# Performance work log

Measured on AMD Instinct MI355X. Metric: run time of the kernel, lower is better.

Reference implementation:

```python
import jax, jax.numpy as jnp
import numpy as np

B, T, DIM, DIM_EPS, H = 4, 1024, 2048, 2048, 16
HD = DIM // H        # 128, value head dim
HDE = DIM_EPS // H   # 128, q/k head dim


def setup_inputs() -> dict:
    key = jax.random.key(0)
    ks = jax.random.split(key, 6)
    s = 0.02
    # rotary frequencies as in llama-style precompute (theta=10000)
    inv_freq = 1.0 / (10000.0 ** (np.arange(0, HDE, 2, dtype=np.float32) / HDE))
    t = np.arange(T, dtype=np.float32)
    ang = np.outer(t, inv_freq)  # (T, HDE//2)
    return {
        "v": jax.random.normal(ks[0], (B, T, DIM), jnp.float32),
        "x_eps": jax.random.normal(ks[1], (B, T, DIM_EPS), jnp.float32),
        "freqs_cos": jnp.asarray(np.cos(ang)),
        "freqs_sin": jnp.asarray(np.sin(ang)),
        "W_eps_attn": jax.random.normal(ks[2], (DIM_EPS, 2 * DIM_EPS), jnp.float32) * s,
        "W_attn": jax.random.normal(ks[3], (DIM, DIM), jnp.float32) * s,
        "W_proj": jax.random.normal(ks[4], (DIM, DIM), jnp.float32) * s,
        "W_eps_proj": jax.random.normal(ks[5], (DIM_EPS, DIM_EPS), jnp.float32) * s,
    }


def _rope(x, cos, sin):
    # x: (B, T, H, HDE) -> complex-multiply by freqs_cis of shape (T, HDE//2)
    xr = x.reshape(*x.shape[:-1], -1, 2)
    x_re, x_im = xr[..., 0], xr[..., 1]
    c = cos[None, :, None, :]  # (1, T, 1, HDE//2)
    s = sin[None, :, None, :]
    o_re = x_re * c - x_im * s
    o_im = x_re * s + x_im * c
    return jnp.stack([o_re, o_im], axis=-1).reshape(x.shape)


def reference(v, x_eps, freqs_cos, freqs_sin, W_eps_attn, W_attn, W_proj, W_eps_proj):
    Bn, Tn, C = v.shape
    qk = x_eps @ W_eps_attn            # (B, T, 2*DIM_EPS)
    q, k = jnp.split(qk, 2, axis=-1)
    vp = v @ W_attn                    # (B, T, DIM)
    q = _rope(q.reshape(Bn, Tn, H, HDE), freqs_cos, freqs_sin)
    k = _rope(k.reshape(Bn, Tn, H, HDE), freqs_cos, freqs_sin)
    q = q.transpose(0, 2, 1, 3)        # (B, H, T, HDE)
    k = k.transpose(0, 2, 1, 3)
    vh = vp.reshape(Bn, Tn, H, HD).transpose(0, 2, 1, 3)
    scale = 1.0 / jnp.sqrt(jnp.asarray(HDE, q.dtype))
    scores = jnp.einsum("bhqd,bhkd->bhqk", q, k) * scale
    causal = jnp.tril(jnp.ones((Tn, Tn), bool))
    scores = jnp.where(causal[None, None], scores, jnp.finfo(scores.dtype).min)
    att = jax.nn.softmax(scores, axis=-1)
    y = jnp.einsum("bhqk,bhkd->bhqd", att, vh)
    y = y.transpose(0, 2, 1, 3).reshape(Bn, Tn, C)
    v_out = y @ W_proj
    x_eps_out = x_eps @ W_eps_proj
    return (v_out, x_eps_out)
```

## Files before the change

kernel.cpp:

```cpp
#include <hip/hip_runtime.h>
#include <stdint.h>

typedef __attribute__((ext_vector_type(8))) short  short8;
typedef __attribute__((ext_vector_type(4))) float  f32x4;
typedef __attribute__((ext_vector_type(4))) float  float4v;
typedef __attribute__((ext_vector_type(4))) unsigned short ushort4v;

#define DEV __device__ __forceinline__

DEV unsigned short f2bf(float f) {
    union { float f; unsigned int u; } x; x.f = f;
    unsigned int u = x.u;
    unsigned int r = (u + 0x7fffu + ((u >> 16) & 1u)) >> 16;
    return (unsigned short)r;
}
DEV float bf2f(unsigned short b) {
    union { unsigned int u; float f; } x; x.u = ((unsigned int)b) << 16;
    return x.f;
}

DEV void gll16(const void* g, void* l) {
    __builtin_amdgcn_global_load_lds(
        (const __attribute__((address_space(1))) void*)g,
        (__attribute__((address_space(3))) void*)l, 16, 0, 0);
}

#define MROWS 4096
#define KDIM  2048
#define NQK   4096

__global__ void cast_f32_bf16(const float* __restrict__ in,
                              unsigned short* __restrict__ out, int n4) {
    int i = blockIdx.x * blockDim.x + threadIdx.x;
    if (i < n4) {
        float4v f = ((const float4v*)in)[i];
        ushort4v o;
        o[0] = f2bf(f[0]); o[1] = f2bf(f[1]); o[2] = f2bf(f[2]); o[3] = f2bf(f[3]);
        ((ushort4v*)out)[i] = o;
    }
}

__global__ void transpose_cast(const float* __restrict__ W,
                               unsigned short* __restrict__ Wt, int K, int N) {
    __shared__ float tile[32][33];
    int tx = threadIdx.x, ty = threadIdx.y;
    int n0 = blockIdx.x * 32, k0 = blockIdx.y * 32;
#pragma unroll
    for (int j = 0; j < 32; j += 8)
        tile[ty + j][tx] = W[(size_t)(k0 + ty + j) * N + n0 + tx];
    __syncthreads();
#pragma unroll
    for (int j = 0; j < 32; j += 8)
        Wt[(size_t)(n0 + ty + j) * K + k0 + tx] = f2bf(tile[tx][ty + j]);
}

__global__ void transpose_v(const unsigned short* __restrict__ vp,
                            unsigned short* __restrict__ vpT) {
    __shared__ unsigned short tile[32][34];
    int tx = threadIdx.x, ty = threadIdx.y;
    int R0 = blockIdx.y * 32;
    int c0 = blockIdx.x * 32;
    int bh = R0 >> 7, d0 = R0 & 127;
    int b = bh >> 4, h = bh & 15;
#pragma unroll
    for (int j = 0; j < 32; j += 8)
        tile[ty + j][tx] = vp[(size_t)(b * 1024 + c0 + ty + j) * 2048 + h * 128 + d0 + tx];
    __syncthreads();
#pragma unroll
    for (int j = 0; j < 32; j += 8)
        vpT[(size_t)(R0 + ty + j) * 1024 + c0 + tx] = tile[tx][ty + j];
}

__global__ __launch_bounds__(512, 2) void gemm256(
    const unsigned short* __restrict__ A0g, const unsigned short* __restrict__ B0g,
    float* __restrict__ Cf0, unsigned short* __restrict__ Ch0,
    int N0, int tx0, int nb0, int outbf0,
    const unsigned short* __restrict__ A1g, const unsigned short* __restrict__ B1g,
    float* __restrict__ Cf1, unsigned short* __restrict__ Ch1,
    int N1, int tx1, int outbf1, int K) {

    __shared__ __align__(16) char lds[131072];

    int blk = blockIdx.x;
    const unsigned short* Ag; const unsigned short* Bg;
    float* Cf; unsigned short* Ch; int N, tx, outbf, nwg;
    if (blk < nb0) { Ag = A0g; Bg = B0g; Cf = Cf0; Ch = Ch0; N = N0; tx = tx0; outbf = outbf0; nwg = nb0; }
    else { blk -= nb0; Ag = A1g; Bg = B1g; Cf = Cf1; Ch = Ch1; N = N1; tx = tx1; outbf = outbf1; nwg = gridDim.x - nb0; }
    { int cpx = nwg >> 3; blk = (blk & 7) * cpx + (blk >> 3); }
    const int bx = blk % tx, by = blk / tx;

    const int tid = threadIdx.x;
    const int lane = tid & 63;
    const int w  = tid >> 6;
    const int lr = lane & 15, lk = lane >> 4;
    const int wm = w >> 2, wn = w & 3;
    const int cswz16 = (lk ^ ((lr >> 3) << 1)) * 16;
    const int rdOff  = lr * 64 + cswz16;
    const int bRow0B = (wn & 1) * 4096;

    const unsigned short* Arow = Ag + (size_t)(by * 256) * K;
    const unsigned short* Brow = Bg + (size_t)(bx * 256) * K;

    const int srow = tid >> 2;
    const int sclog = (tid & 3) ^ (((tid >> 5) & 1) << 1);
    const unsigned short* aSt0 = Arow + (size_t)srow * K + sclog * 8;
    const unsigned short* aSt1 = aSt0 + (size_t)128 * K;
    const unsigned short* bSt0 = Brow + (size_t)srow * K + sclog * 8;
    const unsigned short* bSt1 = bSt0 + (size_t)128 * K;

    char* sA0 = lds;            char* sB0 = lds + 32768;
    char* sA1 = lds + 65536;    char* sB1 = lds + 98304;
    const int sOff = tid * 16;

    const char* aB0 = lds + wm * 16384;
    const char* aB1 = aB0 + 65536;
    const char* bB0 = lds + 32768 + (wn >> 1) * 16384;
    const char* bB1 = bB0 + 65536;

    f32x4 acc[8][4];
#pragma unroll
    for (int m = 0; m < 8; ++m)
#pragma unroll
        for (int n = 0; n < 4; ++n) acc[m][n] = (f32x4){0.f, 0.f, 0.f, 0.f};

    const int NT = K >> 6;

    auto STAGE = [&](const unsigned short* srcHalf, int k0, char* ldsHalf) {
        gll16(srcHalf + k0,      ldsHalf + sOff);
        gll16(srcHalf + k0 + 32, ldsHalf + 8192 + sOff);
    };

    STAGE(aSt0, 0, sA0);  STAGE(aSt1, 0, sA0 + 16384);
    STAGE(bSt0, 0, sB0);  STAGE(bSt1, 0, sB0 + 16384);
    STAGE(aSt0, 64, sA1);
    asm volatile("s_waitcnt vmcnt(2)" ::: "memory");
    __builtin_amdgcn_s_barrier();

#define MFMA_BF(a, b, c) __builtin_amdgcn_mfma_f32_16x16x32_bf16(a, b, c, 0, 0, 0)

#define RD_A(BASE, MH)                                                              \
    _Pragma("unroll") for (int i = 0; i < 4; ++i) {                                 \
        Ar[i][0] = *(const short8*)((BASE) +        (MH) * 4096 + i * 1024 + rdOff); \
        Ar[i][1] = *(const short8*)((BASE) + 8192 + (MH) * 4096 + i * 1024 + rdOff); \
    }

#define RD_B(BASE, NH)                                                                        \
    _Pragma("unroll") for (int j = 0; j < 2; ++j) {                                           \
        Br[j][0] = *(const short8*)((BASE) +        bRow0B + ((NH) * 2 + j) * 1024 + rdOff);  \
        Br[j][1] = *(const short8*)((BASE) + 8192 + bRow0B + ((NH) * 2 + j) * 1024 + rdOff);  \
    }

#define MFMA16(MH, NH)                                                       \
    __builtin_amdgcn_s_setprio(1);                                           \
    _Pragma("unroll") for (int ks = 0; ks < 2; ++ks)                         \
        _Pragma("unroll") for (int i = 0; i < 4; ++i)                        \
            _Pragma("unroll") for (int j = 0; j < 2; ++j)                    \
                acc[(MH) * 4 + i][(NH) * 2 + j] =                            \
                    MFMA_BF(Ar[i][ks], Br[j][ks], acc[(MH) * 4 + i][(NH) * 2 + j]); \
    __builtin_amdgcn_s_setprio(0);

#define PH(RDS, STG, MFMAQ, VMW)                               \
    {                                                          \
        RDS;                                                   \
        STG;                                                   \
        __builtin_amdgcn_s_barrier();                          \
        asm volatile("s_waitcnt lgkmcnt(0)" ::: "memory");     \
        __builtin_amdgcn_sched_barrier(0);                     \
        MFMAQ;                                                 \
        VMW;                                                   \
        __builtin_amdgcn_s_barrier();                          \
    }

#define VMC2 asm volatile("s_waitcnt vmcnt(2)" ::: "memory")

    short8 Ar[4][2], Br[2][2];

    for (int i2 = 0; i2 < NT; i2 += 2) {
        const int kt1 = (i2 + 1) * 64;
        const int kA  = (i2 + 2 < NT ? i2 + 2 : NT - 1) * 64;
        const int kA3 = (i2 + 3 < NT ? i2 + 3 : NT - 1) * 64;

        PH({ RD_A(aB0, 0) RD_B(bB0, 0) },
           { STAGE(aSt1, kt1, sA1 + 16384); STAGE(bSt0, kt1, sB1); STAGE(bSt1, kt1, sB1 + 16384); },
           MFMA16(0, 0), {})
        PH({ RD_B(bB0, 1) }, {}, MFMA16(0, 1), {})
        PH({ RD_A(aB0, 1) RD_B(bB0, 0) }, {}, MFMA16(1, 0), {})
        PH({ RD_B(bB0, 1) },
           { STAGE(aSt0, kA, sA0); },
           MFMA16(1, 1), VMC2)

        PH({ RD_A(aB1, 0) RD_B(bB1, 0) },
           { STAGE(aSt1, kA, sA0 + 16384); STAGE(bSt0, kA, sB0); STAGE(bSt1, kA, sB0 + 16384); },
           MFMA16(0, 0), {})
        PH({ RD_B(bB1, 1) }, {}, MFMA16(0, 1), {})
        PH({ RD_A(aB1, 1) RD_B(bB1, 0) }, {}, MFMA16(1, 0), {})
        PH({ RD_B(bB1, 1) },
           { STAGE(aSt0, kA3, sA1); },
           MFMA16(1, 1), VMC2)
    }
    asm volatile("s_waitcnt vmcnt(0)" ::: "memory");
#undef RD_A
#undef RD_B
#undef MFMA16
#undef PH
#undef VMC2

    if (outbf) {
#pragma unroll
        for (int mf = 0; mf < 8; ++mf)
#pragma unroll
            for (int nf = 0; nf < 4; ++nf)
#pragma unroll
                for (int r = 0; r < 4; ++r) {
                    int row = by * 256 + wm * 128 + mf * 16 + lk * 4 + r;
                    int col = bx * 256 + wn * 64 + nf * 16 + lr;
                    Ch[(size_t)row * N + col] = f2bf(acc[mf][nf][r]);
                }
    } else {
#pragma unroll
        for (int mf = 0; mf < 8; ++mf)
#pragma unroll
            for (int nf = 0; nf < 4; ++nf)
#pragma unroll
                for (int r = 0; r < 4; ++r) {
                    int row = by * 256 + wm * 128 + mf * 16 + lk * 4 + r;
                    int col = bx * 256 + wn * 64 + nf * 16 + lr;
                    Cf[(size_t)row * N + col] = acc[mf][nf][r];
                }
    }
}

__global__ void rope_kernel(unsigned short* __restrict__ qk,
                            const float* __restrict__ fcos,
                            const float* __restrict__ fsin) {
    int idx  = blockIdx.x * 256 + threadIdx.x;
    int row  = idx >> 9;
    int g    = idx & 511;
    int t    = row & 1023;
    int half = g >> 8;
    int hp   = g & 255;
    int h    = hp >> 4;
    int ig   = hp & 15;
    int col  = half * 2048 + h * 128 + ig * 8;
    size_t off = (size_t)row * 4096 + col;

    short8 v = *(short8*)(qk + off);
    int i0 = ig * 4;
    float4v c = *(const float4v*)(fcos + t * 64 + i0);
    float4v s = *(const float4v*)(fsin + t * 64 + i0);
    short8 o;
#pragma unroll
    for (int p = 0; p < 4; ++p) {
        float re = bf2f((unsigned short)v[2 * p]);
        float im = bf2f((unsigned short)v[2 * p + 1]);
        o[2 * p]     = (short)f2bf(re * c[p] - im * s[p]);
        o[2 * p + 1] = (short)f2bf(re * s[p] + im * c[p]);
    }
    *(short8*)(qk + off) = o;
}

__global__ __launch_bounds__(256) void attn_kernel(
    const unsigned short* __restrict__ qk,
    const unsigned short* __restrict__ vpT,
    unsigned short* __restrict__ y) {

    const int bh = blockIdx.x;
    const int qt = 7 - (int)blockIdx.y;
    const int b = bh >> 4, h = bh & 15;
    const int qb0 = qt * 128;

    __shared__ __align__(16) unsigned short Kt[64 * 128];
    __shared__ __align__(16) unsigned short Vt[128 * 64];
    __shared__ __align__(16) unsigned short Pl[4 * 32 * 72];

    const int tid = threadIdx.x, w = tid >> 6, lane = tid & 63;
    const int lr = lane & 15, lk = lane >> 4;

    const unsigned short* Qb = qk + (size_t)(b * 1024) * 4096 + h * 128;
    const unsigned short* Kb = Qb + 2048;
    const unsigned short* Vg = vpT + (size_t)bh * 128 * 1024;
    unsigned short* Pw = &Pl[w * 32 * 72];

    short8 qf[2][4];
#pragma unroll
    for (int m = 0; m < 2; ++m) {
        const unsigned short* qrow = Qb + (size_t)(qb0 + w * 32 + m * 16 + lr) * 4096;
#pragma unroll
        for (int db = 0; db < 4; ++db)
            qf[m][db] = *(const short8*)(qrow + db * 32 + lk * 8);
    }

    f32x4 acc[2][8];
#pragma unroll
    for (int m = 0; m < 2; ++m)
#pragma unroll
        for (int n = 0; n < 8; ++n) acc[m][n] = (f32x4){0.f, 0.f, 0.f, 0.f};
    float m_i[2][4], l_i[2][4];
#pragma unroll
    for (int m = 0; m < 2; ++m)
#pragma unroll
        for (int r = 0; r < 4; ++r) { m_i[m][r] = -1e30f; l_i[m][r] = 0.f; }

    const int nkt = 2 * qt + 2;
    for (int kt = 0; kt < nkt; ++kt) {
#pragma unroll
        for (int c = 0; c < 4; ++c) {
            int base = w * 4096 + c * 1024;
            int row  = (base >> 8) + (lane >> 4);
            int colB = (lane & 15) * 16;
            int scol = colB ^ ((row & 7) << 4);
            gll16(Kb + (size_t)(kt * 64 + row) * 4096 + (scol >> 1),
                  (char*)Kt + base);
        }
#pragma unroll
        for (int c = 0; c < 4; ++c) {
            int base = w * 4096 + c * 1024;
            int d    = (base >> 7) + (lane >> 3);
            int colB = (lane & 7) * 16;
            int scol = colB ^ ((d & 7) << 4);
            gll16(Vg + (size_t)d * 1024 + kt * 64 + (scol >> 1),
                  (char*)Vt + base);
        }
        __syncthreads();

        f32x4 s[2][4];
#pragma unroll
        for (int m = 0; m < 2; ++m)
#pragma unroll
            for (int n = 0; n < 4; ++n) s[m][n] = (f32x4){0.f, 0.f, 0.f, 0.f};
#pragma unroll
        for (int db = 0; db < 4; ++db)
#pragma unroll
            for (int n = 0; n < 4; ++n) {
                int krow = n * 16 + lr;
                int cb = (db * 64 + lk * 16) ^ ((krow & 7) << 4);
                short8 kf = *(const short8*)((const char*)Kt + krow * 256 + cb);
                s[0][n] = __builtin_amdgcn_mfma_f32_16x16x32_bf16(qf[0][db], kf, s[0][n], 0, 0, 0);
                s[1][n] = __builtin_amdgcn_mfma_f32_16x16x32_bf16(qf[1][db], kf, s[1][n], 0, 0, 0);
            }

        const float sc = 0.08838834764831845f;
        const bool diag = (kt >= 2 * qt);
#pragma unroll
        for (int m = 0; m < 2; ++m)
#pragma unroll
            for (int n = 0; n < 4; ++n)
#pragma unroll
                for (int r = 0; r < 4; ++r) {
                    float v = s[m][n][r] * sc;
                    if (diag) {
                        int q   = qb0 + w * 32 + m * 16 + lk * 4 + r;
                        int key = kt * 64 + n * 16 + lr;
                        if (key > q) v = -1e30f;
                    }
                    s[m][n][r] = v;
                }

#pragma unroll
        for (int m = 0; m < 2; ++m) {
            float pm[4];
#pragma unroll
            for (int r = 0; r < 4; ++r)
                pm[r] = fmaxf(fmaxf(s[m][0][r], s[m][1][r]), fmaxf(s[m][2][r], s[m][3][r]));
#pragma unroll
            for (int o = 1; o < 16; o <<= 1)
#pragma unroll
                for (int r = 0; r < 4; ++r)
                    pm[r] = fmaxf(pm[r], __shfl_xor(pm[r], o, 16));

            float resc[4], rs[4];
#pragma unroll
            for (int r = 0; r < 4; ++r) {
                float mn = fmaxf(m_i[m][r], pm[r]);
                resc[r] = __expf(m_i[m][r] - mn);
                m_i[m][r] = mn;
                rs[r] = 0.f;
            }
#pragma unroll
            for (int n = 0; n < 4; ++n)
#pragma unroll
                for (int r = 0; r < 4; ++r) {
                    float p = __expf(s[m][n][r] - m_i[m][r]);
                    s[m][n][r] = p;
                    rs[r] += p;
                }
#pragma unroll
            for (int o = 1; o < 16; o <<= 1)
#pragma unroll
                for (int r = 0; r < 4; ++r)
                    rs[r] += __shfl_xor(rs[r], o, 16);
#pragma unroll
            for (int r = 0; r < 4; ++r)
                l_i[m][r] = l_i[m][r] * resc[r] + rs[r];
#pragma unroll
            for (int n = 0; n < 8; ++n)
#pragma unroll
                for (int r = 0; r < 4; ++r)
                    acc[m][n][r] *= resc[r];

#pragma unroll
            for (int n = 0; n < 4; ++n)
#pragma unroll
                for (int r = 0; r < 4; ++r)
                    Pw[(m * 16 + lk * 4 + r) * 72 + n * 16 + lr] = f2bf(s[m][n][r]);
        }

#pragma unroll
        for (int ks = 0; ks < 2; ++ks) {
            short8 pf0 = *(const short8*)&Pw[(lr) * 72 + ks * 32 + lk * 8];
            short8 pf1 = *(const short8*)&Pw[(16 + lr) * 72 + ks * 32 + lk * 8];
#pragma unroll
            for (int n8 = 0; n8 < 8; ++n8) {
                int d  = n8 * 16 + lr;
                int cb = (ks * 64 + lk * 16) ^ ((d & 7) << 4);
                short8 vf = *(const short8*)((const char*)Vt + d * 128 + cb);
                acc[0][n8] = __builtin_amdgcn_mfma_f32_16x16x32_bf16(pf0, vf, acc[0][n8], 0, 0, 0);
                acc[1][n8] = __builtin_amdgcn_mfma_f32_16x16x32_bf16(pf1, vf, acc[1][n8], 0, 0, 0);
            }
        }
        __syncthreads();
    }

    unsigned short* yb = y + (size_t)(b * 1024) * 2048 + h * 128;
#pragma unroll
    for (int m = 0; m < 2; ++m)
#pragma unroll
        for (int n8 = 0; n8 < 8; ++n8)
#pragma unroll
            for (int r = 0; r < 4; ++r) {
                int t = qb0 + w * 32 + m * 16 + lk * 4 + r;
                int d = n8 * 16 + lr;
                yb[(size_t)t * 2048 + d] = f2bf(acc[m][n8][r] / l_i[m][r]);
            }
}

extern "C" void kernel_launch(void* const* d_in, const int* in_sizes, int n_in,
                              void* d_out, int out_size, void* d_ws, size_t ws_size,
                              hipStream_t stream) {
    const float* v_in  = (const float*)d_in[0];
    const float* xeps  = (const float*)d_in[1];
    const float* fcos  = (const float*)d_in[2];
    const float* fsin  = (const float*)d_in[3];
    const float* Wea   = (const float*)d_in[4];
    const float* Wa    = (const float*)d_in[5];
    const float* Wp    = (const float*)d_in[6];
    const float* Wep   = (const float*)d_in[7];
    float* out = (float*)d_out;

    char* ws = (char*)d_ws;
    unsigned short* xe16 = (unsigned short*)ws;  ws += (size_t)MROWS * KDIM * 2;
    unsigned short* v16  = (unsigned short*)ws;  ws += (size_t)MROWS * KDIM * 2;
    unsigned short* WeaT = (unsigned short*)ws;  ws += (size_t)NQK * KDIM * 2;
    unsigned short* WaT  = (unsigned short*)ws;  ws += (size_t)KDIM * KDIM * 2;
    unsigned short* WpT  = (unsigned short*)ws;  ws += (size_t)KDIM * KDIM * 2;
    unsigned short* WepT = (unsigned short*)ws;  ws += (size_t)KDIM * KDIM * 2;
    unsigned short* qk16 = (unsigned short*)ws;  ws += (size_t)MROWS * NQK * 2;
    unsigned short* vp16 = (unsigned short*)ws;  ws += (size_t)MROWS * KDIM * 2;
    unsigned short* y16  = (unsigned short*)ws;  ws += (size_t)MROWS * KDIM * 2;
    unsigned short* vpT  = v16;

    cast_f32_bf16<<<8192, 256, 0, stream>>>(xeps, xe16, MROWS * KDIM / 4);
    cast_f32_bf16<<<8192, 256, 0, stream>>>(v_in, v16,  MROWS * KDIM / 4);

    transpose_cast<<<dim3(NQK / 32, KDIM / 32), dim3(32, 8), 0, stream>>>(Wea, WeaT, KDIM, NQK);
    transpose_cast<<<dim3(KDIM / 32, KDIM / 32), dim3(32, 8), 0, stream>>>(Wa,  WaT,  KDIM, KDIM);
    transpose_cast<<<dim3(KDIM / 32, KDIM / 32), dim3(32, 8), 0, stream>>>(Wp,  WpT,  KDIM, KDIM);
    transpose_cast<<<dim3(KDIM / 32, KDIM / 32), dim3(32, 8), 0, stream>>>(Wep, WepT, KDIM, KDIM);

    gemm256<<<256, 512, 0, stream>>>(
        xe16, WeaT, nullptr, qk16, NQK, 16, 256, 1,
        xe16, WeaT, nullptr, qk16, NQK, 16, 1, KDIM);

    rope_kernel<<<8192, 256, 0, stream>>>(qk16, fcos, fsin);

    gemm256<<<256, 512, 0, stream>>>(
        v16,  WaT,  nullptr, vp16, KDIM, 8, 128, 1,
        xe16, WepT, out + (size_t)MROWS * KDIM, nullptr, KDIM, 8, 0, KDIM);

    transpose_v<<<dim3(1024 / 32, 8192 / 32), dim3(32, 8), 0, stream>>>(vp16, vpT);

    attn_kernel<<<dim3(64, 8), 256, 0, stream>>>(qk16, vpT, y16);

    gemm256<<<128, 512, 0, stream>>>(
        y16, WpT, out, nullptr, KDIM, 8, 128, 0,
        y16, WpT, out, nullptr, KDIM, 8, 0, KDIM);
}
```

Before: 329.4 us.

## Restructure GEMM pipeline to single-tile prefetch and split-K the output projection

The GEMM main loop changes from a two-tile unrolled schedule with partial vmcnt waits to a per-tile double-buffered loop. It prefetches the whole next K tile at the start of each step, reads fragments between MFMA groups, and waits with vmcnt(0) before reading the next buffer. The final projection GEMM, which used only 128 workgroups, is split along K into two halves across 256 workgroups, writing a partial result into the reused qk buffer, and a new add kernel sums the partials. The occupancy hint on launch_bounds is also dropped. The aim is to fill the GPU for the last GEMM, at the cost of an extra fp32 read/write pass and possibly less overlap in the new loop.

```diff
diff --git a/kernel.cpp b/kernel.cpp
--- a/kernel.cpp
+++ b/kernel.cpp
@@ -40,6 +40,16 @@
     }
 }
 
+__global__ void add_f32(float* __restrict__ out, const float* __restrict__ add, int n4) {
+    int i = blockIdx.x * blockDim.x + threadIdx.x;
+    if (i < n4) {
+        float4v a = ((const float4v*)out)[i];
+        float4v b = ((const float4v*)add)[i];
+        a[0] += b[0]; a[1] += b[1]; a[2] += b[2]; a[3] += b[3];
+        ((float4v*)out)[i] = a;
+    }
+}
+
 __global__ void transpose_cast(const float* __restrict__ W,
                                unsigned short* __restrict__ Wt, int K, int N) {
     __shared__ float tile[32][33];
@@ -71,13 +81,13 @@
         vpT[(size_t)(R0 + ty + j) * 1024 + c0 + tx] = tile[tx][ty + j];
 }
 
-__global__ __launch_bounds__(512, 2) void gemm256(
+__global__ __launch_bounds__(512) void gemm256(
     const unsigned short* __restrict__ A0g, const unsigned short* __restrict__ B0g,
     float* __restrict__ Cf0, unsigned short* __restrict__ Ch0,
     int N0, int tx0, int nb0, int outbf0,
     const unsigned short* __restrict__ A1g, const unsigned short* __restrict__ B1g,
     float* __restrict__ Cf1, unsigned short* __restrict__ Ch1,
-    int N1, int tx1, int outbf1, int K) {
+    int N1, int tx1, int outbf1, int Kst, int Kl) {
 
     __shared__ __align__(16) char lds[131072];
 
@@ -98,15 +108,15 @@
     const int rdOff  = lr * 64 + cswz16;
     const int bRow0B = (wn & 1) * 4096;
 
-    const unsigned short* Arow = Ag + (size_t)(by * 256) * K;
-    const unsigned short* Brow = Bg + (size_t)(bx * 256) * K;
+    const unsigned short* Arow = Ag + (size_t)(by * 256) * Kst;
+    const unsigned short* Brow = Bg + (size_t)(bx * 256) * Kst;
 
     const int srow = tid >> 2;
     const int sclog = (tid & 3) ^ (((tid >> 5) & 1) << 1);
-    const unsigned short* aSt0 = Arow + (size_t)srow * K + sclog * 8;
-    const unsigned short* aSt1 = aSt0 + (size_t)128 * K;
-    const unsigned short* bSt0 = Brow + (size_t)srow * K + sclog * 8;
-    const unsigned short* bSt1 = bSt0 + (size_t)128 * K;
+    const unsigned short* aSt0 = Arow + (size_t)srow * Kst + sclog * 8;
+    const unsigned short* aSt1 = aSt0 + (size_t)128 * Kst;
+    const unsigned short* bSt0 = Brow + (size_t)srow * Kst + sclog * 8;
+    const unsigned short* bSt1 = bSt0 + (size_t)128 * Kst;
 
     char* sA0 = lds;            char* sB0 = lds + 32768;
     char* sA1 = lds + 65536;    char* sB1 = lds + 98304;
@@ -123,23 +133,17 @@
 #pragma unroll
         for (int n = 0; n < 4; ++n) acc[m][n] = (f32x4){0.f, 0.f, 0.f, 0.f};
 
-    const int NT = K >> 6;
+    const int NT = Kl >> 6;
 
     auto STAGE = [&](const unsigned short* srcHalf, int k0, char* ldsHalf) {
         gll16(srcHalf + k0,      ldsHalf + sOff);
         gll16(srcHalf + k0 + 32, ldsHalf + 8192 + sOff);
     };
 
-    STAGE(aSt0, 0, sA0);  STAGE(aSt1, 0, sA0 + 16384);
-    STAGE(bSt0, 0, sB0);  STAGE(bSt1, 0, sB0 + 16384);
-    STAGE(aSt0, 64, sA1);
-    asm volatile("s_waitcnt vmcnt(2)" ::: "memory");
-    __builtin_amdgcn_s_barrier();
-
 #define MFMA_BF(a, b, c) __builtin_amdgcn_mfma_f32_16x16x32_bf16(a, b, c, 0, 0, 0)
 
-#define RD_A(BASE, MH)                                                              \
-    _Pragma("unroll") for (int i = 0; i < 4; ++i) {                                 \
+#define RD_A(BASE, MH)                                                               \
+    _Pragma("unroll") for (int i = 0; i < 4; ++i) {                                  \
         Ar[i][0] = *(const short8*)((BASE) +        (MH) * 4096 + i * 1024 + rdOff); \
         Ar[i][1] = *(const short8*)((BASE) + 8192 + (MH) * 4096 + i * 1024 + rdOff); \
     }
@@ -159,51 +163,61 @@
                     MFMA_BF(Ar[i][ks], Br[j][ks], acc[(MH) * 4 + i][(NH) * 2 + j]); \
     __builtin_amdgcn_s_setprio(0);
 
-#define PH(RDS, STG, MFMAQ, VMW)                               \
-    {                                                          \
-        RDS;                                                   \
-        STG;                                                   \
-        __builtin_amdgcn_s_barrier();                          \
-        asm volatile("s_waitcnt lgkmcnt(0)" ::: "memory");     \
-        __builtin_amdgcn_sched_barrier(0);                     \
-        MFMAQ;                                                 \
-        VMW;                                                   \
-        __builtin_amdgcn_s_barrier();                          \
-    }
-
-#define VMC2 asm volatile("s_waitcnt vmcnt(2)" ::: "memory")
+#define LGKM0 asm volatile("s_waitcnt lgkmcnt(0)" ::: "memory"); \
+              __builtin_amdgcn_sched_barrier(0)
+#define BARR  __builtin_amdgcn_s_barrier()
 
     short8 Ar[4][2], Br[2][2];
 
-    for (int i2 = 0; i2 < NT; i2 += 2) {
-        const int kt1 = (i2 + 1) * 64;
-        const int kA  = (i2 + 2 < NT ? i2 + 2 : NT - 1) * 64;
-        const int kA3 = (i2 + 3 < NT ? i2 + 3 : NT - 1) * 64;
-
-        PH({ RD_A(aB0, 0) RD_B(bB0, 0) },
-           { STAGE(aSt1, kt1, sA1 + 16384); STAGE(bSt0, kt1, sB1); STAGE(bSt1, kt1, sB1 + 16384); },
-           MFMA16(0, 0), {})
-        PH({ RD_B(bB0, 1) }, {}, MFMA16(0, 1), {})
-        PH({ RD_A(aB0, 1) RD_B(bB0, 0) }, {}, MFMA16(1, 0), {})
-        PH({ RD_B(bB0, 1) },
-           { STAGE(aSt0, kA, sA0); },
-           MFMA16(1, 1), VMC2)
-
-        PH({ RD_A(aB1, 0) RD_B(bB1, 0) },
-           { STAGE(aSt1, kA, sA0 + 16384); STAGE(bSt0, kA, sB0); STAGE(bSt1, kA, sB0 + 16384); },
-           MFMA16(0, 0), {})
-        PH({ RD_B(bB1, 1) }, {}, MFMA16(0, 1), {})
-        PH({ RD_A(aB1, 1) RD_B(bB1, 0) }, {}, MFMA16(1, 0), {})
-        PH({ RD_B(bB1, 1) },
-           { STAGE(aSt0, kA3, sA1); },
-           MFMA16(1, 1), VMC2)
-    }
+    STAGE(aSt0, 0, sA0);  STAGE(aSt1, 0, sA0 + 16384);
+    STAGE(bSt0, 0, sB0);  STAGE(bSt1, 0, sB0 + 16384);
     asm volatile("s_waitcnt vmcnt(0)" ::: "memory");
+    BARR;
+    RD_A(aB0, 0)
+    RD_B(bB0, 0)
+
+    for (int u = 0; u < NT; ++u) {
+        const bool par = u & 1;
+        const char* aC = par ? aB1 : aB0;
+        const char* bC = par ? bB1 : bB0;
+        const char* aN = par ? aB0 : aB1;
+        const char* bN = par ? bB0 : bB1;
+        char* dA = par ? sA0 : sA1;
+        char* dB = par ? sB0 : sB1;
+        const int kN = (u + 1 < NT ? u + 1 : NT - 1) * 64;
+
+        STAGE(aSt0, kN, dA);  STAGE(aSt1, kN, dA + 16384);
+        STAGE(bSt0, kN, dB);  STAGE(bSt1, kN, dB + 16384);
+        BARR;
+        LGKM0;
+        MFMA16(0, 0)
+        RD_B(bC, 1)
+        BARR;
+
+        LGKM0;
+        MFMA16(0, 1)
+        RD_A(aC, 1)
+        RD_B(bC, 0)
+        BARR;
+
+        LGKM0;
+        MFMA16(1, 0)
+        RD_B(bC, 1)
+        BARR;
+
+        LGKM0;
+        MFMA16(1, 1)
+        asm volatile("s_waitcnt vmcnt(0)" ::: "memory");
+        RD_A(aN, 0)
+        RD_B(bN, 0)
+        BARR;
+    }
+    asm volatile("s_waitcnt lgkmcnt(0)" ::: "memory");
 #undef RD_A
 #undef RD_B
 #undef MFMA16
-#undef PH
-#undef VMC2
+#undef LGKM0
+#undef BARR
 
     if (outbf) {
 #pragma unroll
@@ -458,6 +472,7 @@
     unsigned short* vp16 = (unsigned short*)ws;  ws += (size_t)MROWS * KDIM * 2;
     unsigned short* y16  = (unsigned short*)ws;  ws += (size_t)MROWS * KDIM * 2;
     unsigned short* vpT  = v16;
+    float* projP = (float*)qk16;
 
     cast_f32_bf16<<<8192, 256, 0, stream>>>(xeps, xe16, MROWS * KDIM / 4);
     cast_f32_bf16<<<8192, 256, 0, stream>>>(v_in, v16,  MROWS * KDIM / 4);
@@ -469,19 +484,21 @@
 
     gemm256<<<256, 512, 0, stream>>>(
         xe16, WeaT, nullptr, qk16, NQK, 16, 256, 1,
-        xe16, WeaT, nullptr, qk16, NQK, 16, 1, KDIM);
+        xe16, WeaT, nullptr, qk16, NQK, 16, 1, KDIM, KDIM);
 
     rope_kernel<<<8192, 256, 0, stream>>>(qk16, fcos, fsin);
 
     gemm256<<<256, 512, 0, stream>>>(
         v16,  WaT,  nullptr, vp16, KDIM, 8, 128, 1,
-        xe16, WepT, out + (size_t)MROWS * KDIM, nullptr, KDIM, 8, 0, KDIM);
+        xe16, WepT, out + (size_t)MROWS * KDIM, nullptr, KDIM, 8, 0, KDIM, KDIM);
 
     transpose_v<<<dim3(1024 / 32, 8192 / 32), dim3(32, 8), 0, stream>>>(vp16, vpT);
 
     attn_kernel<<<dim3(64, 8), 256, 0, stream>>>(qk16, vpT, y16);
 
-    gemm256<<<128, 512, 0, stream>>>(
-        y16, WpT, out, nullptr, KDIM, 8, 128, 0,
-        y16, WpT, out, nullptr, KDIM, 8, 0, KDIM);
-}
+    gemm256<<<256, 512, 0, stream>>>(
+        y16,        WpT,        out,   nullptr, KDIM, 8, 128, 0,
+        y16 + 1024, WpT + 1024, projP, nullptr, KDIM, 8, 0, KDIM, 1024);
+
+    add_f32<<<8192, 256, 0, stream>>>(out, projP, MROWS * KDIM / 4);
+}
```

New measurement: 332.2 us. No clear change (+0.8%).
